# Kernel optimization log

Measured on AMD Instinct MI355X. Metric: run time of the kernel, lower is better.

Reference implementation:

```python
import jax, jax.numpy as jnp
import numpy as np

RAD = 4   # corr lookup radius
NH, NP = 8, 4  # deform attn heads / points (single level)


def conv2d(x, w, b, pad):
    y = jax.lax.conv_general_dilated(x, w, (1, 1), [(pad, pad), (pad, pad)],
                                     dimension_numbers=('NCHW', 'OIHW', 'NCHW'))
    return y + b[None, :, None, None]


def bilinear_gather(imgf, H, W, px, py):
    # imgf: [N, C, H*W]; px, py: [N, P] pixel coords; zero padding (grid_sample 'zeros')
    x0 = jnp.floor(px); y0 = jnp.floor(py)
    wx = px - x0; wy = py - y0
    def tap(xi, yi, wt):
        valid = (xi >= 0) & (xi <= W - 1) & (yi >= 0) & (yi <= H - 1)
        idx = (jnp.clip(yi, 0, H - 1) * W + jnp.clip(xi, 0, W - 1)).astype(jnp.int32)
        v = jnp.take_along_axis(imgf, idx[:, None, :], axis=2)
        return v * (wt * valid)[:, None, :]
    return (tap(x0, y0, (1 - wx) * (1 - wy)) + tap(x0 + 1, y0, wx * (1 - wy))
            + tap(x0, y0 + 1, (1 - wx) * wy) + tap(x0 + 1, y0 + 1, wx * wy))


def sine_pos_embed(B, H, W, npf, temperature=10000.0):
    # PositionEmbeddingSine with normalize=True
    scale = 2.0 * np.pi; eps = 1e-6
    y = jnp.broadcast_to(jnp.arange(1, H + 1, dtype=jnp.float32)[:, None], (H, W))
    x = jnp.broadcast_to(jnp.arange(1, W + 1, dtype=jnp.float32)[None, :], (H, W))
    y = (y - 0.5) / (H + eps) * scale
    x = (x - 0.5) / (W + eps) * scale
    dim_t = temperature ** (2.0 * (jnp.arange(npf) // 2).astype(jnp.float32) / npf)
    px = x[..., None] / dim_t
    py = y[..., None] / dim_t
    px = jnp.stack([jnp.sin(px[..., 0::2]), jnp.cos(px[..., 1::2])], -1).reshape(H, W, npf)
    py = jnp.stack([jnp.sin(py[..., 0::2]), jnp.cos(py[..., 1::2])], -1).reshape(H, W, npf)
    pos = jnp.concatenate([py, px], -1)
    return jnp.broadcast_to(pos[None], (B, H, W, 2 * npf)).reshape(B, H * W, 2 * npf)


def layer_norm(x, g, b):
    m = x.mean(-1, keepdims=True)
    v = ((x - m) ** 2).mean(-1, keepdims=True)
    return (x - m) / jnp.sqrt(v + 1e-5) * g + b


def _forward(fmap1, fmap2, flow, wc1, bc1, wc2, bc2, wf1, bf1, wf2, bf2, wcf, bcf,
             wfh1, bfh1, wfh2, bfh2, w_off, b_off, w_aw, b_aw, w_val, b_val,
             w_out, b_out, ln1_g, ln1_b, w_ff1, b_ff1, w_ff2, b_ff2, ln2_g, ln2_b):
    B, C, H, W = fmap1.shape
    HW = H * W
    dh = C // NH
    relu = jax.nn.relu
    # ---- CorrBlock.corr: all-pairs correlation volume ----
    corr = jnp.einsum('bcq,bck->bqk', fmap1.reshape(B, C, HW), fmap2.reshape(B, C, HW))
    corr = corr / jnp.sqrt(jnp.asarray(C, jnp.float32))
    corrf = corr.reshape(B * HW, 1, HW)  # [B*HW, 1, H2*W2]
    # ---- correlation lookup at coords = base grid + flow (bilinear, align_corners=True) ----
    gy, gx = jnp.meshgrid(jnp.arange(H, dtype=jnp.float32),
                          jnp.arange(W, dtype=jnp.float32), indexing='ij')
    cx = (gx[None] + flow[:, 0]).reshape(B * HW)
    cy = (gy[None] + flow[:, 1]).reshape(B * HW)
    d = jnp.linspace(-RAD, RAD, 2 * RAD + 1)
    oy, ox = jnp.meshgrid(d, d, indexing='ij')  # RAFT quirk: delta[...,0]=dy, delta[...,1]=dx
    px = cx[:, None] + oy.reshape(-1)[None, :]
    py = cy[:, None] + ox.reshape(-1)[None, :]
    corr_feat = bilinear_gather(corrf, H, W, px, py).reshape(B, H, W, (2 * RAD + 1) ** 2)
    corr_feat = corr_feat.transpose(0, 3, 1, 2)  # [B, 81, H, W]
    # ---- BasicMotionEncoder + FlowHead (BasicUpdateBlock.forward path) ----
    cor = relu(conv2d(corr_feat, wc1, bc1, 0))
    cor = relu(conv2d(cor, wc2, bc2, 1))
    flo = relu(conv2d(flow, wf1, bf1, 3))
    flo = relu(conv2d(flo, wf2, bf2, 1))
    mf = relu(conv2d(jnp.concatenate([cor, flo], 1), wcf, bcf, 1))
    mf = jnp.concatenate([mf, flow], 1)  # [B,128,H,W]
    delta_flow = conv2d(relu(conv2d(mf, wfh1, bfh1, 1)), wfh2, bfh2, 1)  # [B,2,H,W]
    # ---- single-level MSDeformAttn encoder layer over fmap1 tokens ----
    src = fmap1.reshape(B, C, HW).transpose(0, 2, 1)  # [B, Lq, C]
    pos = sine_pos_embed(B, H, W, C // 2)
    q = src + pos
    off = (q @ w_off.T + b_off).reshape(B, HW, NH, 1, NP, 2)
    aw = jax.nn.softmax((q @ w_aw.T + b_aw).reshape(B, HW, NH, NP), axis=-1)
    val = (src @ w_val.T + b_val).reshape(B, HW, NH, dh)
    ref = jnp.stack([(gx.reshape(-1) + 0.5) / W, (gy.reshape(-1) + 0.5) / H], -1)  # [HW,2]
    loc = (ref[None, :, None, None, None, :] + off / jnp.asarray([W, H], jnp.float32))[:, :, :, 0]
    # normalized loc -> pixel coords with align_corners=False convention
    px2 = (loc[..., 0] * W - 0.5).transpose(0, 2, 1, 3).reshape(B * NH, HW * NP)
    py2 = (loc[..., 1] * H - 0.5).transpose(0, 2, 1, 3).reshape(B * NH, HW * NP)
    vflat = val.transpose(0, 2, 3, 1).reshape(B * NH, dh, HW)
    samp = bilinear_gather(vflat, H, W, px2, py2).reshape(B, NH, dh, HW, NP)
    attn = (samp * aw.transpose(0, 2, 1, 3)[:, :, None]).sum(-1)  # [B,NH,dh,HW]
    attn = attn.transpose(0, 3, 1, 2).reshape(B, HW, C) @ w_out.T + b_out
    src = layer_norm(src + attn, ln1_g, ln1_b)
    ff = jax.nn.relu(src @ w_ff1.T + b_ff1) @ w_ff2.T + b_ff2
    src = layer_norm(src + ff, ln2_g, ln2_b)
    return src, delta_flow


def setup_inputs():
    key = jax.random.key(0)
    ks = jax.random.split(key, 20)
    B, C, H, W = 4, 256, 48, 48
    def w(i, shape, s=0.02):
        return jax.random.normal(ks[i], shape, jnp.float32) * s
    return {
        'fmap1': jax.random.normal(ks[0], (B, C, H, W), jnp.float32),
        'fmap2': jax.random.normal(ks[1], (B, C, H, W), jnp.float32),
        'flow': jax.random.normal(ks[2], (B, 2, H, W), jnp.float32),
        'wc1': w(3, (256, 81, 1, 1)), 'bc1': jnp.zeros((256,)),
        'wc2': w(4, (192, 256, 3, 3)), 'bc2': jnp.zeros((192,)),
        'wf1': w(5, (128, 2, 7, 7)), 'bf1': jnp.zeros((128,)),
        'wf2': w(6, (64, 128, 3, 3)), 'bf2': jnp.zeros((64,)),
        'wcf': w(7, (126, 256, 3, 3)), 'bcf': jnp.zeros((126,)),
        'wfh1': w(8, (256, 128, 3, 3)), 'bfh1': jnp.zeros((256,)),
        'wfh2': w(9, (2, 256, 3, 3)), 'bfh2': jnp.zeros((2,)),
        'w_off': w(10, (64, 256)), 'b_off': jnp.zeros((64,)),
        'w_aw': w(11, (32, 256)), 'b_aw': jnp.zeros((32,)),
        'w_val': w(12, (256, 256)), 'b_val': jnp.zeros((256,)),
        'w_out': w(13, (256, 256)), 'b_out': jnp.zeros((256,)),
        'ln1_g': jnp.ones((256,)), 'ln1_b': jnp.zeros((256,)),
        'w_ff1': w(14, (1024, 256)), 'b_ff1': jnp.zeros((1024,)),
        'w_ff2': w(15, (256, 1024)), 'b_ff2': jnp.zeros((256,)),
        'ln2_g': jnp.ones((256,)), 'ln2_b': jnp.zeros((256,)),
    }


def reference(fmap1, fmap2, flow, wc1, bc1, wc2, bc2, wf1, bf1, wf2, bf2, wcf, bcf,
              wfh1, bfh1, wfh2, bfh2, w_off, b_off, w_aw, b_aw, w_val, b_val,
              w_out, b_out, ln1_g, ln1_b, w_ff1, b_ff1, w_ff2, b_ff2, ln2_g, ln2_b):
    return _forward(fmap1, fmap2, flow, wc1, bc1, wc2, bc2, wf1, bf1, wf2, bf2, wcf, bcf,
                    wfh1, bfh1, wfh2, bfh2, w_off, b_off, w_aw, b_aw, w_val, b_val,
                    w_out, b_out, ln1_g, ln1_b, w_ff1, b_ff1, w_ff2, b_ff2, ln2_g, ln2_b)
```

## Files before the change

### kernel.cpp

```cpp
#include <hip/hip_runtime.h>
#include <hip/hip_bf16.h>
#include <math.h>

#define HH 48
#define WW 48
#define HW 2304
#define BB 4
#define CC 256

typedef __hip_bfloat16 bf16;
typedef __attribute__((ext_vector_type(8))) short s8v;
typedef __attribute__((ext_vector_type(4))) float f4v;

__device__ inline float bf2f(short u) {
  unsigned v = ((unsigned)(unsigned short)u) << 16;
  return __builtin_bit_cast(float, v);
}

__global__ __launch_bounds__(256) void prep_k(const float* __restrict__ fmap1,
                                              const float* __restrict__ fmap2,
                                              float* __restrict__ srcT,
                                              bf16* __restrict__ f1t,
                                              bf16* __restrict__ qb,
                                              bf16* __restrict__ f2t) {
  __shared__ float t[64][65];
  int z = blockIdx.z;
  int p0 = blockIdx.x * 64, c0 = blockIdx.y * 64;
  int b = z & 3;
  const float* src = (z < 4) ? fmap2 : fmap1;
  const float* inb = src + ((size_t)b * CC + c0) * HW + p0;
#pragma unroll
  for (int i = 0; i < 16; ++i) {
    int idx = threadIdx.x + i * 256;
    int c = idx >> 6, p = idx & 63;
    t[c][p] = inb[(size_t)c * HW + p];
  }
  __syncthreads();
  if (z < 4) {
    bf16* ob = f2t + ((size_t)b * HW + p0) * 256 + c0;
#pragma unroll
    for (int i = 0; i < 16; ++i) {
      int idx = threadIdx.x + i * 256;
      int p = idx >> 6, c = idx & 63;
      ob[(size_t)p * 256 + c] = (bf16)t[c][p];
    }
  } else {
    const float TWO_PI = 6.283185307179586f;
#pragma unroll
    for (int i = 0; i < 16; ++i) {
      int idx = threadIdx.x + i * 256;
      int pl = idx >> 6, cl = idx & 63;
      int c = c0 + cl;
      int p = p0 + pl;
      int y = p / WW, x = p % WW;
      float s = t[cl][pl];
      int axis = c >> 7;
      int cc = c & 127;
      int mm = cc >> 1;
      float coord = (axis ? ((float)x + 0.5f) : ((float)y + 0.5f)) * (TWO_PI / (48.f + 1e-6f));
      float tp = exp2f((float)mm * (13.287712379549449f / 64.f));
      float a = coord / tp;
      float pv = (cc & 1) ? cosf(a) : sinf(a);
      size_t o = ((size_t)b * HW + p) * 256 + c;
      srcT[o] = s;
      f1t[o] = (bf16)s;
      qb[o] = (bf16)(s + pv);
    }
  }
}

__global__ __launch_bounds__(256) void corr_mfma_k(const bf16* __restrict__ f1t,
                                                   const bf16* __restrict__ f2t,
                                                   bf16* __restrict__ corr) {
  int b = blockIdx.z;
  int m0 = blockIdx.y * 128, n0 = blockIdx.x * 64;
  __shared__ short As[128][64];
  __shared__ short Bs[64][64];
  int tid = threadIdx.x;
  int arl = tid >> 1, asl = (tid & 1) * 4;
  int brl = tid >> 2, bsl = (tid & 3) * 2;
  int wave = tid >> 6, lane = tid & 63;
  int wm = (wave >> 1) * 64, wn = (wave & 1) * 32;
  int fl = lane & 15, fk8 = lane >> 4;
  f4v acc[4][2] = {};
  const bf16* arow = f1t + ((size_t)b * HW + m0 + arl) * 256;
  const bf16* brow = f2t + ((size_t)b * HW + n0 + brl) * 256;
#pragma unroll
  for (int c0 = 0; c0 < 256; c0 += 64) {
#pragma unroll
    for (int q = 0; q < 4; ++q) {
      int sr = asl + q;
      *(uint4*)&As[arl][((sr ^ (arl & 7))) * 8] = *(const uint4*)(arow + c0 + sr * 8);
    }
#pragma unroll
    for (int q = 0; q < 2; ++q) {
      int sr = bsl + q;
      *(uint4*)&Bs[brl][((sr ^ (brl & 7))) * 8] = *(const uint4*)(brow + c0 + sr * 8);
    }
    __syncthreads();
#pragma unroll
    for (int cc = 0; cc < 2; ++cc) {
      s8v af[4], bfr[2];
#pragma unroll
      for (int i = 0; i < 4; ++i) {
        int ar = wm + i * 16 + fl;
        af[i] = *(const s8v*)&As[ar][(((cc * 4 + fk8) ^ (ar & 7))) * 8];
      }
#pragma unroll
      for (int j = 0; j < 2; ++j) {
        int br = wn + j * 16 + fl;
        bfr[j] = *(const s8v*)&Bs[br][(((cc * 4 + fk8) ^ (br & 7))) * 8];
      }
#pragma unroll
      for (int i = 0; i < 4; ++i)
#pragma unroll
        for (int j = 0; j < 2; ++j)
          acc[i][j] = __builtin_amdgcn_mfma_f32_16x16x32_bf16(af[i], bfr[j], acc[i][j], 0, 0, 0);
    }
    __syncthreads();
  }
  bf16* outp = corr + ((size_t)b * HW + m0) * HW + n0;
#pragma unroll
  for (int j = 0; j < 2; ++j) {
    int o = wn + j * 16 + fl;
#pragma unroll
    for (int i = 0; i < 4; ++i)
#pragma unroll
      for (int r = 0; r < 4; ++r) {
        int m = wm + i * 16 + fk8 * 4 + r;
        outp[(size_t)m * HW + o] = (bf16)(acc[i][j][r] * 0.0625f);
      }
  }
}

__global__ __launch_bounds__(256) void corr_lookup_k(const bf16* __restrict__ corr,
                                                     const float* __restrict__ flow,
                                                     bf16* __restrict__ cf) {
  int g = blockIdx.x * 256 + threadIdx.x;
  int t = g % 96;
  int n = g / 96;
  if (t >= 81) { cf[g] = (bf16)0.f; return; }
  int b = n / HW;
  int p = n % HW;
  int y = p / WW, x = p % WW;
  float fx = flow[((size_t)b * 2 + 0) * HW + p];
  float fy = flow[((size_t)b * 2 + 1) * HW + p];
  float px = (float)x + fx + (float)(t / 9 - 4);
  float py = (float)y + fy + (float)(t % 9 - 4);
  const bf16* row = corr + (size_t)n * HW;
  float x0f = floorf(px), y0f = floorf(py);
  int x0 = (int)x0f, y0 = (int)y0f;
  float wx = px - x0f, wy = py - y0f;
  float acc = 0.f;
  if ((unsigned)x0 < WW && (unsigned)y0 < HH) acc += (float)row[y0 * WW + x0] * (1.f - wx) * (1.f - wy);
  if ((unsigned)(x0 + 1) < WW && (unsigned)y0 < HH) acc += (float)row[y0 * WW + x0 + 1] * wx * (1.f - wy);
  if ((unsigned)x0 < WW && (unsigned)(y0 + 1) < HH) acc += (float)row[(y0 + 1) * WW + x0] * (1.f - wx) * wy;
  if ((unsigned)(x0 + 1) < WW && (unsigned)(y0 + 1) < HH) acc += (float)row[(y0 + 1) * WW + x0 + 1] * wx * wy;
  cf[g] = (bf16)acc;
}

struct WtSegs {
  const float* src[12];
  unsigned dstOff[12];
  int Cout[12], Cin[12], KP[12], KS2[12];
  unsigned cum[13];
};

__global__ __launch_bounds__(256) void wt_all_k(WtSegs s, bf16* __restrict__ base) {
  unsigned idx = blockIdx.x * 256 + threadIdx.x;
  if (idx >= s.cum[12]) return;
  int seg = 0;
#pragma unroll
  for (int i = 1; i < 12; ++i)
    if (idx >= s.cum[i]) seg = i;
  unsigned r = idx - s.cum[seg];
  int KP = s.KP[seg], Cout = s.Cout[seg], Cin = s.Cin[seg], KS2 = s.KS2[seg];
  int c = r % KP;
  int o = (r / KP) % Cout;
  int t = r / (KP * Cout);
  float v;
  if (KS2 == 0) {
    int cc = c >> 6, tt = c & 63;
    v = (tt < 49) ? s.src[seg][((size_t)o * 2 + cc) * 49 + tt] : 0.f;
  } else {
    v = (c < Cin) ? s.src[seg][((size_t)o * Cin + c) * KS2 + t] : 0.f;
  }
  base[s.dstOff[seg] + r] = (bf16)v;
}

__global__ __launch_bounds__(256) void im2col7_k(const float* __restrict__ flow,
                                                 bf16* __restrict__ col7) {
  int g = blockIdx.x * 256 + threadIdx.x;
  int kp = g & 127;
  int n = g >> 7;
  int b = n / HW;
  int p = n % HW;
  int y = p / WW, x = p % WW;
  int cc = kp >> 6, tt = kp & 63;
  float v = 0.f;
  if (tt < 49) {
    int ky = tt / 7, kx = tt % 7;
    int yy = y + ky - 3, xx = x + kx - 3;
    if ((unsigned)yy < (unsigned)HH && (unsigned)xx < (unsigned)WW)
      v = flow[((size_t)b * 2 + cc) * HW + yy * WW + xx];
  }
  col7[g] = (bf16)v;
}

struct GSegs {
  const bf16* in[4];
  const bf16* wt[4];
  const float* bias[4];
  const float* bias2[4];
  float* outf[4];
  bf16* outb[4];
  int split[4], O[4], KP[4], taps[4], OStride[4], OOff[4], relu[4], nTn[4];
  int blkStart[4];
  int nseg;
};

__global__ __launch_bounds__(256) void gemm_group_k(GSegs s) {
  int blk = blockIdx.x;
  int seg = 0;
#pragma unroll
  for (int i = 1; i < 4; ++i)
    if (i < s.nseg && blk >= s.blkStart[i]) seg = i;
  int rel = blk - s.blkStart[seg];
  int nTn = s.nTn[seg];
  int bm = rel / nTn, bn = rel % nTn;
  int m0 = bm * 128, n0 = bn * 64;
  int KP = s.KP[seg], O = s.O[seg], taps = s.taps[seg];
  const bf16* in = s.in[seg];
  const bf16* wt = s.wt[seg];

  __shared__ short As[128][64];
  __shared__ short Bs[64][64];
  int tid = threadIdx.x;
  int arl = tid >> 1, asl = (tid & 1) * 4;
  int brl = tid >> 2, bsl = (tid & 3) * 2;
  int wave = tid >> 6, lane = tid & 63;
  int wm = (wave >> 1) * 64, wn = (wave & 1) * 32;
  int fl = lane & 15, fk8 = lane >> 4;
  f4v acc[4][2] = {};
  int m = m0 + arl;
  int b = m / HW;
  int p = m - b * HW;
  int y = p / WW, x = p - y * WW;
  int wo = n0 + brl;
  bool wvalid = wo < O;
  int wo_c = wvalid ? wo : 0;
  for (int t = 0; t < taps; ++t) {
    int yy = y, xx = x;
    bool valid = true;
    if (taps == 9) {
      int ky = t / 3, kx = t - ky * 3;
      yy = y + ky - 1;
      xx = x + kx - 1;
      valid = ((unsigned)yy < (unsigned)HH) & ((unsigned)xx < (unsigned)WW);
    }
    const bf16* arow = in + ((size_t)b * HW + yy * WW + xx) * KP;
    const bf16* wrow = wt + ((size_t)t * O + wo_c) * KP;
    for (int c0 = 0; c0 < KP; c0 += 64) {
#pragma unroll
      for (int q = 0; q < 4; ++q) {
        int sr = asl + q;
        uint4 av = {0u, 0u, 0u, 0u};
        if (valid && (c0 + sr * 8) < KP) av = *(const uint4*)(arow + c0 + sr * 8);
        *(uint4*)&As[arl][((sr ^ (arl & 7))) * 8] = av;
      }
#pragma unroll
      for (int q = 0; q < 2; ++q) {
        int sr = bsl + q;
        uint4 bv = {0u, 0u, 0u, 0u};
        if (wvalid && (c0 + sr * 8) < KP) bv = *(const uint4*)(wrow + c0 + sr * 8);
        *(uint4*)&Bs[brl][((sr ^ (brl & 7))) * 8] = bv;
      }
      __syncthreads();
#pragma unroll
      for (int cc = 0; cc < 2; ++cc) {
        s8v af[4], bfr[2];
#pragma unroll
        for (int i = 0; i < 4; ++i) {
          int ar = wm + i * 16 + fl;
          af[i] = *(const s8v*)&As[ar][(((cc * 4 + fk8) ^ (ar & 7))) * 8];
        }
#pragma unroll
        for (int j = 0; j < 2; ++j) {
          int br = wn + j * 16 + fl;
          bfr[j] = *(const s8v*)&Bs[br][(((cc * 4 + fk8) ^ (br & 7))) * 8];
        }
#pragma unroll
        for (int i = 0; i < 4; ++i)
#pragma unroll
          for (int j = 0; j < 2; ++j)
            acc[i][j] = __builtin_amdgcn_mfma_f32_16x16x32_bf16(af[i], bfr[j], acc[i][j], 0, 0, 0);
      }
      __syncthreads();
    }
  }
  int OStride = s.OStride[seg], OOff = s.OOff[seg], relu = s.relu[seg], split = s.split[seg];
  const float* bias = s.bias[seg];
  const float* bias2 = s.bias2[seg];
  float* outf = s.outf[seg];
  bf16* outb = s.outb[seg];
#pragma unroll
  for (int j = 0; j < 2; ++j) {
    int o = n0 + wn + j * 16 + fl;
    if (o < O) {
      float bsv = (bias2 != nullptr && o >= split) ? bias2[o - split] : bias[o];
#pragma unroll
      for (int i = 0; i < 4; ++i)
#pragma unroll
        for (int r = 0; r < 4; ++r) {
          int mm = m0 + wm + i * 16 + fk8 * 4 + r;
          float v = acc[i][j][r] + bsv;
          if (relu) v = fmaxf(v, 0.f);
          if (outb) outb[(size_t)mm * OStride + OOff + o] = (bf16)v;
          else outf[(size_t)mm * OStride + OOff + o] = v;
        }
    }
  }
}

__global__ __launch_bounds__(256) void convfh2_k(const bf16* __restrict__ fh1,
                                                 const float* __restrict__ w,
                                                 const float* __restrict__ bias,
                                                 float* __restrict__ out) {
  __shared__ float wl[4608];
  int tid = threadIdx.x;
#pragma unroll
  for (int i = tid; i < 4608; i += 256) {
    int o2 = i & 1;
    int t = (i >> 1) % 9;
    int c = i / 18;
    wl[i] = w[((size_t)o2 * 256 + c) * 9 + t];
  }
  __syncthreads();
  int wave = tid >> 6, lane = tid & 63;
  int pix = blockIdx.x * 4 + wave;
  int b = pix / HW;
  int q = pix % HW;
  int y = q / WW, x = q % WW;
  int c0 = lane * 4;
  float a0 = 0.f, a1 = 0.f;
#pragma unroll
  for (int ky = 0; ky < 3; ++ky) {
    int yy = y + ky - 1;
    if ((unsigned)yy >= (unsigned)HH) continue;
#pragma unroll
    for (int kx = 0; kx < 3; ++kx) {
      int xx = x + kx - 1;
      if ((unsigned)xx >= (unsigned)WW) continue;
      int t = ky * 3 + kx;
      const bf16* row = fh1 + ((size_t)b * HW + yy * WW + xx) * 256 + c0;
      ushort4 v = *(const ushort4*)row;
      unsigned short vv[4] = {v.x, v.y, v.z, v.w};
#pragma unroll
      for (int j = 0; j < 4; ++j) {
        float fv = bf2f((short)vv[j]);
        float2 wp = *(const float2*)&wl[((c0 + j) * 9 + t) * 2];
        a0 += fv * wp.x;
        a1 += fv * wp.y;
      }
    }
  }
#pragma unroll
  for (int offl = 32; offl > 0; offl >>= 1) {
    a0 += __shfl_xor(a0, offl);
    a1 += __shfl_xor(a1, offl);
  }
  if (lane == 0) {
    out[(size_t)b * 2 * HW + q] = a0 + bias[0];
    out[((size_t)b * 2 + 1) * HW + q] = a1 + bias[1];
  }
}

__global__ void copy_flow_k(const float* __restrict__ flow, bf16* __restrict__ mf) {
  int g = blockIdx.x * 256 + threadIdx.x;
  int p = g % HW;
  int c = (g / HW) % 2;
  int b = g / (2 * HW);
  mf[((size_t)b * HW + p) * 128 + 126 + c] = (bf16)flow[g];
}

__global__ __launch_bounds__(256) void deform_k(const float* __restrict__ val,
                                                const float* __restrict__ oa,
                                                bf16* __restrict__ attn) {
  int g = blockIdx.x * 256 + threadIdx.x;
  int d = g & 31;
  int nh = g >> 5;
  int h = nh & 7;
  int n = nh >> 3;
  int b = n / HW;
  int p = n % HW;
  int y = p / WW, x = p % WW;
  const float* ap = oa + (size_t)n * 96 + 64 + h * 4;
  float l0 = ap[0], l1 = ap[1], l2 = ap[2], l3 = ap[3];
  float mx = fmaxf(fmaxf(l0, l1), fmaxf(l2, l3));
  float e0 = expf(l0 - mx), e1 = expf(l1 - mx), e2 = expf(l2 - mx), e3 = expf(l3 - mx);
  float inv = 1.f / (e0 + e1 + e2 + e3);
  float wts[4] = {e0 * inv, e1 * inv, e2 * inv, e3 * inv};
  const float* offp = oa + (size_t)n * 96 + h * 8;
  const float* vb = val + (size_t)b * HW * 256 + h * 32 + d;
  float acc = 0.f;
#pragma unroll
  for (int pt = 0; pt < 4; ++pt) {
    float ox = offp[pt * 2 + 0];
    float oy = offp[pt * 2 + 1];
    float w = wts[pt];
    float px = (float)x + ox, py = (float)y + oy;
    float x0f = floorf(px), y0f = floorf(py);
    int x0 = (int)x0f, y0 = (int)y0f;
    float wx = px - x0f, wy = py - y0f;
    float s = 0.f;
    if ((unsigned)x0 < WW && (unsigned)y0 < HH)
      s += vb[(size_t)(y0 * WW + x0) * 256] * (1.f - wx) * (1.f - wy);
    if ((unsigned)(x0 + 1) < WW && (unsigned)y0 < HH)
      s += vb[(size_t)(y0 * WW + x0 + 1) * 256] * wx * (1.f - wy);
    if ((unsigned)x0 < WW && (unsigned)(y0 + 1) < HH)
      s += vb[(size_t)((y0 + 1) * WW + x0) * 256] * (1.f - wx) * wy;
    if ((unsigned)(x0 + 1) < WW && (unsigned)(y0 + 1) < HH)
      s += vb[(size_t)((y0 + 1) * WW + x0 + 1) * 256] * wx * wy;
    acc += w * s;
  }
  attn[(size_t)n * 256 + h * 32 + d] = (bf16)acc;
}

__global__ __launch_bounds__(256) void ln_add_k(const float* __restrict__ A,
                                                const float* __restrict__ Bv,
                                                const float* __restrict__ g,
                                                const float* __restrict__ be,
                                                float* __restrict__ out,
                                                bf16* __restrict__ outb) {
  int n = blockIdx.x;
  int c = threadIdx.x;
  float v = A[(size_t)n * 256 + c] + Bv[(size_t)n * 256 + c];
  float s1 = v, s2 = v * v;
#pragma unroll
  for (int o = 32; o > 0; o >>= 1) {
    s1 += __shfl_down(s1, o);
    s2 += __shfl_down(s2, o);
  }
  __shared__ float r1[4], r2[4], mv[2];
  int wid = c >> 6, lane = c & 63;
  if (lane == 0) {
    r1[wid] = s1;
    r2[wid] = s2;
  }
  __syncthreads();
  if (c == 0) {
    float a = r1[0] + r1[1] + r1[2] + r1[3];
    float q2 = r2[0] + r2[1] + r2[2] + r2[3];
    float mean = a * (1.f / 256.f);
    mv[0] = mean;
    mv[1] = q2 * (1.f / 256.f) - mean * mean;
  }
  __syncthreads();
  float mean = mv[0], var = mv[1];
  float r = (v - mean) * rsqrtf(var + 1e-5f) * g[c] + be[c];
  out[(size_t)n * 256 + c] = r;
  if (outb) outb[(size_t)n * 256 + c] = (bf16)r;
}

extern "C" void kernel_launch(void* const* d_in, const int* in_sizes, int n_in,
                              void* d_out, int out_size, void* d_ws, size_t ws_size,
                              hipStream_t stream) {
  const float* fmap1 = (const float*)d_in[0];
  const float* fmap2 = (const float*)d_in[1];
  const float* flow = (const float*)d_in[2];
  const float* wc1 = (const float*)d_in[3];
  const float* bc1 = (const float*)d_in[4];
  const float* wc2 = (const float*)d_in[5];
  const float* bc2 = (const float*)d_in[6];
  const float* wf1 = (const float*)d_in[7];
  const float* bf1 = (const float*)d_in[8];
  const float* wf2 = (const float*)d_in[9];
  const float* bf2 = (const float*)d_in[10];
  const float* wcf = (const float*)d_in[11];
  const float* bcf = (const float*)d_in[12];
  const float* wfh1 = (const float*)d_in[13];
  const float* bfh1 = (const float*)d_in[14];
  const float* wfh2 = (const float*)d_in[15];
  const float* bfh2 = (const float*)d_in[16];
  const float* w_off = (const float*)d_in[17];
  const float* b_off = (const float*)d_in[18];
  const float* w_aw = (const float*)d_in[19];
  const float* b_aw = (const float*)d_in[20];
  const float* w_val = (const float*)d_in[21];
  const float* b_val = (const float*)d_in[22];
  const float* w_out = (const float*)d_in[23];
  const float* b_out = (const float*)d_in[24];
  const float* ln1_g = (const float*)d_in[25];
  const float* ln1_b = (const float*)d_in[26];
  const float* w_ff1 = (const float*)d_in[27];
  const float* b_ff1 = (const float*)d_in[28];
  const float* w_ff2 = (const float*)d_in[29];
  const float* b_ff2 = (const float*)d_in[30];
  const float* ln2_g = (const float*)d_in[31];
  const float* ln2_b = (const float*)d_in[32];

  float* ws = (float*)d_ws;
  float* out_src = (float*)d_out;
  float* out_df = out_src + (size_t)BB * HW * CC;

  const size_t F_WT = 0;
  const size_t F_CORR = 1000000;
  const size_t F_F1T = 11700000;
  const size_t F_F2T = 12900000;
  const size_t F_QB = 14100000;
  const size_t F_SRCT = 15300000;
  const size_t F_CF = 17700000;
  const size_t F_COL7 = 18200000;
  const size_t F_COR1 = 18800000;
  const size_t F_FLO1 = 20000000;
  const size_t F_CAT = 20600000;
  const size_t F_MF = 21800000;
  const size_t F_FH1 = 22400000;
  const size_t F_OA = 23600000;
  const size_t F_VAL = 24500000;
  const size_t F_ATTN = 26900000;
  const size_t F_TMP = 28100000;
  const size_t F_SRC1 = 30500000;
  const size_t F_SRC1B = 32900000;
  const size_t F_FF1 = 34100000;
  const size_t F_FF2 = 38900000;

  bf16* wkbase = (bf16*)(ws + F_WT);
  bf16* wk1 = wkbase + 0;
  bf16* wk2 = wkbase + 24576;
  bf16* wkf2 = wkbase + 466944;
  bf16* wkcf = wkbase + 540672;
  bf16* wkfh1 = wkbase + 830976;
  bf16* wl_oa = wkbase + 1125888;
  bf16* wl_val = wkbase + 1150464;
  bf16* wl_out = wkbase + 1216000;
  bf16* wl_ff1 = wkbase + 1281536;
  bf16* wl_ff2 = wkbase + 1543680;
  bf16* wk7 = wkbase + 1805824;
  bf16* corrb = (bf16*)(ws + F_CORR);
  bf16* f1t = (bf16*)(ws + F_F1T);
  bf16* f2t = (bf16*)(ws + F_F2T);
  bf16* qb = (bf16*)(ws + F_QB);
  bf16* cf = (bf16*)(ws + F_CF);
  bf16* col7 = (bf16*)(ws + F_COL7);
  bf16* cor1 = (bf16*)(ws + F_COR1);
  bf16* flo1 = (bf16*)(ws + F_FLO1);
  bf16* cat = (bf16*)(ws + F_CAT);
  bf16* mf = (bf16*)(ws + F_MF);
  bf16* fh1 = (bf16*)(ws + F_FH1);
  bf16* attnb = (bf16*)(ws + F_ATTN);
  bf16* src1b = (bf16*)(ws + F_SRC1B);
  bf16* ff1b = (bf16*)(ws + F_FF1);

  WtSegs segs;
  const float* srcs[12] = {wc1, wc2, wf2, wcf, wfh1, w_off, w_aw, w_val, w_out, w_ff1, w_ff2, wf1};
  unsigned offs[12] = {0, 24576, 466944, 540672, 830976, 1125888, 1142272, 1150464, 1216000, 1281536, 1543680, 1805824};
  int couts[12] = {256, 192, 64, 126, 256, 64, 32, 256, 256, 1024, 256, 128};
  int cins[12] = {81, 256, 128, 256, 128, 256, 256, 256, 256, 256, 1024, 2};
  int kps[12] = {96, 256, 128, 256, 128, 256, 256, 256, 256, 256, 1024, 128};
  int ks2[12] = {1, 9, 9, 9, 9, 1, 1, 1, 1, 1, 1, 0};
  unsigned cum = 0;
  for (int i = 0; i < 12; ++i) {
    segs.src[i] = srcs[i];
    segs.dstOff[i] = offs[i];
    segs.Cout[i] = couts[i];
    segs.Cin[i] = cins[i];
    segs.KP[i] = kps[i];
    segs.KS2[i] = ks2[i];
    segs.cum[i] = cum;
    cum += (unsigned)((ks2[i] ? ks2[i] : 1) * couts[i] * kps[i]);
  }
  segs.cum[12] = cum;
  wt_all_k<<<dim3((cum + 255) / 256), 256, 0, stream>>>(segs, wkbase);

  prep_k<<<dim3(36, 4, 8), 256, 0, stream>>>(fmap1, fmap2, ws + F_SRCT, f1t, qb, f2t);
  im2col7_k<<<dim3(4608), 256, 0, stream>>>(flow, col7);
  copy_flow_k<<<dim3(72), 256, 0, stream>>>(flow, mf);

  corr_mfma_k<<<dim3(36, 18, 4), 256, 0, stream>>>(f1t, f2t, corrb);
  corr_lookup_k<<<dim3(3456), 256, 0, stream>>>(corrb, flow, cf);

  auto setseg = [](GSegs& G, int i, const bf16* in, const bf16* wt, const float* bias,
                   const float* bias2, int split, float* outf, bf16* outb, int O, int KP,
                   int taps, int OStride, int OOff, int relu) {
    G.in[i] = in; G.wt[i] = wt; G.bias[i] = bias; G.bias2[i] = bias2; G.split[i] = split;
    G.outf[i] = outf; G.outb[i] = outb; G.O[i] = O; G.KP[i] = KP; G.taps[i] = taps;
    G.OStride[i] = OStride; G.OOff[i] = OOff; G.relu[i] = relu;
    G.nTn[i] = (O + 63) / 64;
  };
  auto finseg = [](GSegs& G, int n) {
    int cumb = 0;
    for (int i = 0; i < 4; ++i) {
      if (i < n) { G.blkStart[i] = cumb; cumb += G.nTn[i] * 72; }
      else G.blkStart[i] = 0x7fffffff;
    }
    G.nseg = n;
    return cumb;
  };

  GSegs GA;
  setseg(GA, 0, cf, wk1, bc1, nullptr, 1 << 30, nullptr, cor1, 256, 96, 1, 256, 0, 1);
  setseg(GA, 1, col7, wk7, bf1, nullptr, 1 << 30, nullptr, flo1, 128, 128, 1, 128, 0, 1);
  setseg(GA, 2, qb, wl_oa, b_off, b_aw, 64, ws + F_OA, nullptr, 96, 256, 1, 96, 0, 0);
  setseg(GA, 3, f1t, wl_val, b_val, nullptr, 1 << 30, ws + F_VAL, nullptr, 256, 256, 1, 256, 0, 0);
  int nblkA = finseg(GA, 4);
  gemm_group_k<<<dim3(nblkA), 256, 0, stream>>>(GA);

  deform_k<<<dim3(9216), 256, 0, stream>>>(ws + F_VAL, ws + F_OA, attnb);

  GSegs GB;
  setseg(GB, 0, cor1, wk2, bc2, nullptr, 1 << 30, nullptr, cat, 192, 256, 9, 256, 0, 1);
  setseg(GB, 1, flo1, wkf2, bf2, nullptr, 1 << 30, nullptr, cat, 64, 128, 9, 256, 192, 1);
  setseg(GB, 2, attnb, wl_out, b_out, nullptr, 1 << 30, ws + F_TMP, nullptr, 256, 256, 1, 256, 0, 0);
  int nblkB = finseg(GB, 3);
  gemm_group_k<<<dim3(nblkB), 256, 0, stream>>>(GB);

  ln_add_k<<<dim3(9216), 256, 0, stream>>>(ws + F_TMP, ws + F_SRCT, ln1_g, ln1_b, ws + F_SRC1, src1b);

  GSegs GC;
  setseg(GC, 0, cat, wkcf, bcf, nullptr, 1 << 30, nullptr, mf, 126, 256, 9, 128, 0, 1);
  setseg(GC, 1, src1b, wl_ff1, b_ff1, nullptr, 1 << 30, nullptr, ff1b, 1024, 256, 1, 1024, 0, 1);
  int nblkC = finseg(GC, 2);
  gemm_group_k<<<dim3(nblkC), 256, 0, stream>>>(GC);

  GSegs GD;
  setseg(GD, 0, mf, wkfh1, bfh1, nullptr, 1 << 30, nullptr, fh1, 256, 128, 9, 256, 0, 1);
  setseg(GD, 1, ff1b, wl_ff2, b_ff2, nullptr, 1 << 30, ws + F_FF2, nullptr, 256, 1024, 1, 256, 0, 0);
  int nblkD = finseg(GD, 2);
  gemm_group_k<<<dim3(nblkD), 256, 0, stream>>>(GD);

  convfh2_k<<<dim3(2304), 256, 0, stream>>>(fh1, wfh2, bfh2, out_df);
  ln_add_k<<<dim3(9216), 256, 0, stream>>>(ws + F_FF2, ws + F_SRC1, ln2_g, ln2_b, out_src, nullptr);

  (void)in_sizes; (void)n_in; (void)out_size; (void)ws_size;
}
```

Baseline: 300.3 us.

## Double-buffer LDS tiles with register prefetch in corr and grouped GEMM kernels

```diff
diff --git a/kernel.cpp b/kernel.cpp
--- a/kernel.cpp
+++ b/kernel.cpp
@@ -74,8 +74,8 @@
                                                    bf16* __restrict__ corr) {
   int b = blockIdx.z;
   int m0 = blockIdx.y * 128, n0 = blockIdx.x * 64;
-  __shared__ short As[128][64];
-  __shared__ short Bs[64][64];
+  __shared__ short As[2][128][64];
+  __shared__ short Bs[2][64][64];
   int tid = threadIdx.x;
   int arl = tid >> 1, asl = (tid & 1) * 4;
   int brl = tid >> 2, bsl = (tid & 3) * 2;
@@ -85,17 +85,29 @@
   f4v acc[4][2] = {};
   const bf16* arow = f1t + ((size_t)b * HW + m0 + arl) * 256;
   const bf16* brow = f2t + ((size_t)b * HW + n0 + brl) * 256;
-#pragma unroll
-  for (int c0 = 0; c0 < 256; c0 += 64) {
+  uint4 apre[4], bpre[2];
+#pragma unroll
+  for (int q = 0; q < 4; ++q) apre[q] = *(const uint4*)(arow + (asl + q) * 8);
+#pragma unroll
+  for (int q = 0; q < 2; ++q) bpre[q] = *(const uint4*)(brow + (bsl + q) * 8);
+  int cur = 0;
+  for (int st = 0; st < 4; ++st) {
 #pragma unroll
     for (int q = 0; q < 4; ++q) {
       int sr = asl + q;
-      *(uint4*)&As[arl][((sr ^ (arl & 7))) * 8] = *(const uint4*)(arow + c0 + sr * 8);
+      *(uint4*)&As[cur][arl][((sr ^ (arl & 7))) * 8] = apre[q];
     }
 #pragma unroll
     for (int q = 0; q < 2; ++q) {
       int sr = bsl + q;
-      *(uint4*)&Bs[brl][((sr ^ (brl & 7))) * 8] = *(const uint4*)(brow + c0 + sr * 8);
+      *(uint4*)&Bs[cur][brl][((sr ^ (brl & 7))) * 8] = bpre[q];
+    }
+    if (st < 3) {
+      int c0 = (st + 1) * 64;
+#pragma unroll
+      for (int q = 0; q < 4; ++q) apre[q] = *(const uint4*)(arow + c0 + (asl + q) * 8);
+#pragma unroll
+      for (int q = 0; q < 2; ++q) bpre[q] = *(const uint4*)(brow + c0 + (bsl + q) * 8);
     }
     __syncthreads();
 #pragma unroll
@@ -104,12 +116,12 @@
 #pragma unroll
       for (int i = 0; i < 4; ++i) {
         int ar = wm + i * 16 + fl;
-        af[i] = *(const s8v*)&As[ar][(((cc * 4 + fk8) ^ (ar & 7))) * 8];
+        af[i] = *(const s8v*)&As[cur][ar][(((cc * 4 + fk8) ^ (ar & 7))) * 8];
       }
 #pragma unroll
       for (int j = 0; j < 2; ++j) {
         int br = wn + j * 16 + fl;
-        bfr[j] = *(const s8v*)&Bs[br][(((cc * 4 + fk8) ^ (br & 7))) * 8];
+        bfr[j] = *(const s8v*)&Bs[cur][br][(((cc * 4 + fk8) ^ (br & 7))) * 8];
       }
 #pragma unroll
       for (int i = 0; i < 4; ++i)
@@ -117,7 +129,7 @@
         for (int j = 0; j < 2; ++j)
           acc[i][j] = __builtin_amdgcn_mfma_f32_16x16x32_bf16(af[i], bfr[j], acc[i][j], 0, 0, 0);
     }
-    __syncthreads();
+    cur ^= 1;
   }
   bf16* outp = corr + ((size_t)b * HW + m0) * HW + n0;
 #pragma unroll
@@ -233,8 +245,8 @@
   const bf16* in = s.in[seg];
   const bf16* wt = s.wt[seg];
 
-  __shared__ short As[128][64];
-  __shared__ short Bs[64][64];
+  __shared__ short As[2][128][64];
+  __shared__ short Bs[2][64][64];
   int tid = threadIdx.x;
   int arl = tid >> 1, asl = (tid & 1) * 4;
   int brl = tid >> 2, bsl = (tid & 3) * 2;
@@ -249,7 +261,14 @@
   int wo = n0 + brl;
   bool wvalid = wo < O;
   int wo_c = wvalid ? wo : 0;
-  for (int t = 0; t < taps; ++t) {
+
+  int nc0 = (KP + 63) >> 6;
+  int S = taps * nc0;
+  uint4 apre[4], bpre[2];
+
+  auto load_stage = [&](int st) {
+    int t = st / nc0;
+    int c0 = (st - t * nc0) * 64;
     int yy = y, xx = x;
     bool valid = true;
     if (taps == 9) {
@@ -260,43 +279,57 @@
     }
     const bf16* arow = in + ((size_t)b * HW + yy * WW + xx) * KP;
     const bf16* wrow = wt + ((size_t)t * O + wo_c) * KP;
-    for (int c0 = 0; c0 < KP; c0 += 64) {
-#pragma unroll
-      for (int q = 0; q < 4; ++q) {
-        int sr = asl + q;
-        uint4 av = {0u, 0u, 0u, 0u};
-        if (valid && (c0 + sr * 8) < KP) av = *(const uint4*)(arow + c0 + sr * 8);
-        *(uint4*)&As[arl][((sr ^ (arl & 7))) * 8] = av;
+#pragma unroll
+    for (int q = 0; q < 4; ++q) {
+      int col = c0 + (asl + q) * 8;
+      uint4 v = {0u, 0u, 0u, 0u};
+      if (valid && col < KP) v = *(const uint4*)(arow + col);
+      apre[q] = v;
+    }
+#pragma unroll
+    for (int q = 0; q < 2; ++q) {
+      int col = c0 + (bsl + q) * 8;
+      uint4 v = {0u, 0u, 0u, 0u};
+      if (wvalid && col < KP) v = *(const uint4*)(wrow + col);
+      bpre[q] = v;
+    }
+  };
+
+  load_stage(0);
+  int cur = 0;
+  for (int st = 0; st < S; ++st) {
+#pragma unroll
+    for (int q = 0; q < 4; ++q) {
+      int sr = asl + q;
+      *(uint4*)&As[cur][arl][((sr ^ (arl & 7))) * 8] = apre[q];
+    }
+#pragma unroll
+    for (int q = 0; q < 2; ++q) {
+      int sr = bsl + q;
+      *(uint4*)&Bs[cur][brl][((sr ^ (brl & 7))) * 8] = bpre[q];
+    }
+    if (st + 1 < S) load_stage(st + 1);
+    __syncthreads();
+#pragma unroll
+    for (int cc = 0; cc < 2; ++cc) {
+      s8v af[4], bfr[2];
+#pragma unroll
+      for (int i = 0; i < 4; ++i) {
+        int ar = wm + i * 16 + fl;
+        af[i] = *(const s8v*)&As[cur][ar][(((cc * 4 + fk8) ^ (ar & 7))) * 8];
       }
 #pragma unroll
-      for (int q = 0; q < 2; ++q) {
-        int sr = bsl + q;
-        uint4 bv = {0u, 0u, 0u, 0u};
-        if (wvalid && (c0 + sr * 8) < KP) bv = *(const uint4*)(wrow + c0 + sr * 8);
-        *(uint4*)&Bs[brl][((sr ^ (brl & 7))) * 8] = bv;
+      for (int j = 0; j < 2; ++j) {
+        int br = wn + j * 16 + fl;
+        bfr[j] = *(const s8v*)&Bs[cur][br][(((cc * 4 + fk8) ^ (br & 7))) * 8];
       }
-      __syncthreads();
-#pragma unroll
-      for (int cc = 0; cc < 2; ++cc) {
-        s8v af[4], bfr[2];
-#pragma unroll
-        for (int i = 0; i < 4; ++i) {
-          int ar = wm + i * 16 + fl;
-          af[i] = *(const s8v*)&As[ar][(((cc * 4 + fk8) ^ (ar & 7))) * 8];
-        }
-#pragma unroll
-        for (int j = 0; j < 2; ++j) {
-          int br = wn + j * 16 + fl;
-          bfr[j] = *(const s8v*)&Bs[br][(((cc * 4 + fk8) ^ (br & 7))) * 8];
-        }
-#pragma unroll
-        for (int i = 0; i < 4; ++i)
-#pragma unroll
-          for (int j = 0; j < 2; ++j)
-            acc[i][j] = __builtin_amdgcn_mfma_f32_16x16x32_bf16(af[i], bfr[j], acc[i][j], 0, 0, 0);
-      }
-      __syncthreads();
-    }
+#pragma unroll
+      for (int i = 0; i < 4; ++i)
+#pragma unroll
+        for (int j = 0; j < 2; ++j)
+          acc[i][j] = __builtin_amdgcn_mfma_f32_16x16x32_bf16(af[i], bfr[j], acc[i][j], 0, 0, 0);
+    }
+    cur ^= 1;
   }
   int OStride = s.OStride[seg], OOff = s.OOff[seg], relu = s.relu[seg], split = s.split[seg];
   const float* bias = s.bias[seg];
```

New measurement: 286.0 us. -4.8%, faster.
